# Kernel tuning notes

Measured on AMD Instinct MI355X. Metric: run time of the kernel, lower is better.

Reference implementation:

```python
import jax, jax.numpy as jnp
import numpy as np

N_NODES = 50000
N_EDGES = 800000
H = 4


def setup_inputs() -> dict:
    key = jax.random.key(0)
    ks = jax.random.split(key, 12)
    s = 0.05
    return {
        "x_feat": jax.random.normal(ks[0], (N_NODES, 128), jnp.float32),
        "W_fc": jax.random.normal(ks[1], (128, 256), jnp.float32) * s,
        "W1": jax.random.normal(ks[2], (256, 256), jnp.float32) * s,
        "al1": jax.random.normal(ks[3], (H, 64), jnp.float32) * s,
        "ar1": jax.random.normal(ks[4], (H, 64), jnp.float32) * s,
        "b1": jnp.zeros((256,), jnp.float32),
        "W2": jax.random.normal(ks[5], (256, 256), jnp.float32) * s,
        "al2": jax.random.normal(ks[6], (H, 64), jnp.float32) * s,
        "ar2": jax.random.normal(ks[7], (H, 64), jnp.float32) * s,
        "b2": jnp.zeros((256,), jnp.float32),
        "src": jax.random.randint(ks[8], (N_EDGES,), 0, N_NODES, jnp.int64 if jax.config.jax_enable_x64 else jnp.int32),
        "dst": jax.random.randint(ks[9], (N_EDGES,), 0, N_NODES, jnp.int64 if jax.config.jax_enable_x64 else jnp.int32),
    }


def _gat_layer(x, src, dst, W, attn_l, attn_r, bias, n_nodes):
    """DGL GATConv: project, per-edge leaky-relu scores, edge softmax by dst,
    weighted segment-sum, + bias, ELU. Returns [N, H, dh]."""
    h, dh = attn_l.shape
    feat = (x @ W).reshape(n_nodes, h, dh)            # [N,H,dh]
    el = jnp.einsum('nhd,hd->nh', feat, attn_l)        # [N,H]
    er = jnp.einsum('nhd,hd->nh', feat, attn_r)        # [N,H]
    e = jax.nn.leaky_relu(el[src] + er[dst], 0.2)      # [E,H]
    # numerically stable segment softmax over incoming edges of each dst
    m = jax.ops.segment_max(e, dst, num_segments=n_nodes)
    ex = jnp.exp(e - m[dst])
    z = jax.ops.segment_sum(ex, dst, num_segments=n_nodes)
    a = ex / z[dst]                                    # [E,H]
    msg = feat[src] * a[:, :, None]                    # [E,H,dh]
    out = jax.ops.segment_sum(msg, dst, num_segments=n_nodes)  # [N,H,dh]
    out = out + bias.reshape(h, dh)
    return jax.nn.elu(out)


def reference(x_feat, W_fc, W1, al1, ar1, b1, W2, al2, ar2, b2, src, dst):
    n = x_feat.shape[0]
    h = jnp.tanh(x_feat @ W_fc)                         # [N,256] (dropout = identity in eval)
    g1 = _gat_layer(h, src, dst, W1, al1, ar1, b1, n)   # [N,4,64]
    g1 = g1.reshape(n, -1)                              # [N,256]
    g2 = _gat_layer(g1, src, dst, W2, al2, ar2, b2, n)  # [N,4,64]
    return jnp.mean(g2, axis=-2)                        # mean over heads -> [N,64]
```

## Files before the change

kernel.cpp:

```cpp
#include <hip/hip_runtime.h>
#include <hip/hip_bf16.h>
#include <hip/hip_fp16.h>
#include <math.h>


typedef __attribute__((ext_vector_type(8))) short bf16x8;
typedef __attribute__((ext_vector_type(4))) float f32x4;

typedef const __attribute__((address_space(1))) char gas_char;
typedef __attribute__((address_space(3))) char las_char;

__device__ __forceinline__ void gload16(const void* g, void* l) {
    __builtin_amdgcn_global_load_lds((gas_char*)g, (las_char*)l, 16, 0, 0);
}

__device__ __forceinline__ void split2(float v, short& h, short& l) {
    __hip_bfloat16 bh = __float2bfloat16(v);
    float r = v - __bfloat162float(bh);
    __hip_bfloat16 bl = __float2bfloat16(r);
    h = *reinterpret_cast<short*>(&bh);
    l = *reinterpret_cast<short*>(&bl);
}

__device__ __forceinline__ float fast_tanh(float x) {
    x = fminf(fmaxf(x, -15.f), 15.f);
    float e = __expf(2.f * x);
    return (e - 1.f) * __builtin_amdgcn_rcpf(e + 1.f);
}

__device__ __forceinline__ float leaky02(float x) { return x > 0.f ? x : 0.2f * x; }

__device__ __forceinline__ float sel_head(float4 q, int h) {
    float lo = (h & 1) ? q.y : q.x;
    float hi = (h & 1) ? q.w : q.z;
    return (h & 2) ? hi : lo;
}

__global__ __launch_bounds__(256) void wsplit3_kernel(
        const float* __restrict__ W0, short* __restrict__ B0h, short* __restrict__ B0l,
        const float* __restrict__ W1, short* __restrict__ B1h, short* __restrict__ B1l,
        const float* __restrict__ W2, short* __restrict__ B2h, short* __restrict__ B2l) {
    int idx = blockIdx.x * 256 + threadIdx.x;
    const float* W;
    short *Bh, *Bl;
    int K, rel;
    if (idx < 128 * 256) {
        W = W0; Bh = B0h; Bl = B0l; K = 128; rel = idx;
    } else if (idx < 128 * 256 + 256 * 256) {
        W = W1; Bh = B1h; Bl = B1l; K = 256; rel = idx - 128 * 256;
    } else if (idx < 128 * 256 + 2 * 256 * 256) {
        W = W2; Bh = B2h; Bl = B2l; K = 256; rel = idx - 128 * 256 - 256 * 256;
    } else {
        return;
    }
    int k = rel >> 8, n = rel & 255;
    short h, l;
    split2(W[rel], h, l);
    Bh[n * K + k] = h;
    Bl[n * K + k] = l;
}

__global__ __launch_bounds__(256) void xsplit_kernel(const float* __restrict__ X,
                                                     short* __restrict__ Xh,
                                                     short* __restrict__ Xl, int total) {
    int idx = blockIdx.x * 256 + threadIdx.x;
    if (idx >= total) return;
    short h, l;
    split2(X[idx], h, l);
    Xh[idx] = h;
    Xl[idx] = l;
}

template<int K, bool TANH, bool ELER, bool SPLIT_OUT>
__global__ __launch_bounds__(256, 2) void mfma_gemm_kernel(
        const short* __restrict__ Ah, const short* __restrict__ Al,
        const short* __restrict__ Bh, const short* __restrict__ Bl,
        short* __restrict__ Oh, short* __restrict__ Ol, __half* __restrict__ O16,
        int M,
        const float* __restrict__ al, const float* __restrict__ ar,
        float* __restrict__ el, float* __restrict__ er) {
    __shared__ __align__(16) short As_h[2][128 * 32];
    __shared__ __align__(16) short As_l[2][128 * 32];
    __shared__ __align__(16) short Bs_h[2][128 * 32];
    __shared__ __align__(16) short Bs_l[2][128 * 32];

    const int tid = threadIdx.x;
    const int row0 = blockIdx.x * 128;
    const int col0 = blockIdx.y * 128;

    const int lane = tid & 63;
    const int lr = lane & 15;
    const int lg = lane >> 4;
    const int wid = tid >> 6;
    const int wm = wid >> 1;
    const int wn = wid & 1;

    const int srow = wid * 32 + (lane >> 2);
    const int scol = (lane & 3) * 8;
    const size_t aoff1 = (size_t)(row0 + srow) * K + scol;
    const size_t aoff2 = aoff1 + (size_t)16 * K;
    const size_t boff1 = (size_t)(col0 + srow) * K + scol;
    const size_t boff2 = boff1 + (size_t)16 * K;
    const int lbase1 = (wid * 32) * 32;
    const int lbase2 = (wid * 32 + 16) * 32;

    auto stage = [&](int buf, int k0) {
        gload16(Ah + aoff1 + k0, &As_h[buf][lbase1]);
        gload16(Ah + aoff2 + k0, &As_h[buf][lbase2]);
        gload16(Al + aoff1 + k0, &As_l[buf][lbase1]);
        gload16(Al + aoff2 + k0, &As_l[buf][lbase2]);
        gload16(Bh + boff1 + k0, &Bs_h[buf][lbase1]);
        gload16(Bh + boff2 + k0, &Bs_h[buf][lbase2]);
        gload16(Bl + boff1 + k0, &Bs_l[buf][lbase1]);
        gload16(Bl + boff2 + k0, &Bs_l[buf][lbase2]);
    };

    f32x4 acc[4][4];
#pragma unroll
    for (int i = 0; i < 4; ++i)
#pragma unroll
        for (int j = 0; j < 4; ++j) acc[i][j] = (f32x4){0.f, 0.f, 0.f, 0.f};

    constexpr int NT = K / 32;
    stage(0, 0);
    __syncthreads();

    int cur = 0;
#pragma unroll
    for (int t = 0; t < NT; ++t) {
        if (t + 1 < NT) stage(cur ^ 1, (t + 1) * 32);

        bf16x8 ah[4], av[4], bh[4], bv[4];
#pragma unroll
        for (int q = 0; q < 4; ++q) {
            int arow = (wm * 64 + q * 16 + lr) * 32 + lg * 8;
            int brow = (wn * 64 + q * 16 + lr) * 32 + lg * 8;
            ah[q] = *reinterpret_cast<const bf16x8*>(&As_h[cur][arow]);
            av[q] = *reinterpret_cast<const bf16x8*>(&As_l[cur][arow]);
            bh[q] = *reinterpret_cast<const bf16x8*>(&Bs_h[cur][brow]);
            bv[q] = *reinterpret_cast<const bf16x8*>(&Bs_l[cur][brow]);
        }
#pragma unroll
        for (int mt = 0; mt < 4; ++mt)
#pragma unroll
            for (int nt = 0; nt < 4; ++nt) {
                acc[mt][nt] = __builtin_amdgcn_mfma_f32_16x16x32_bf16(ah[mt], bh[nt], acc[mt][nt], 0, 0, 0);
                acc[mt][nt] = __builtin_amdgcn_mfma_f32_16x16x32_bf16(ah[mt], bv[nt], acc[mt][nt], 0, 0, 0);
                acc[mt][nt] = __builtin_amdgcn_mfma_f32_16x16x32_bf16(av[mt], bh[nt], acc[mt][nt], 0, 0, 0);
            }
        __syncthreads();
        cur ^= 1;
    }

    const int head = blockIdx.y * 2 + wn;
    float alv[4], arv[4];
    if (ELER) {
#pragma unroll
        for (int nt = 0; nt < 4; ++nt) {
            alv[nt] = al[head * 64 + nt * 16 + lr];
            arv[nt] = ar[head * 64 + nt * 16 + lr];
        }
    }
#pragma unroll
    for (int mt = 0; mt < 4; ++mt) {
#pragma unroll
        for (int r = 0; r < 4; ++r) {
            int row = row0 + wm * 64 + mt * 16 + lg * 4 + r;
            bool valid = row < M;
            float sl = 0.f, sr_ = 0.f;
#pragma unroll
            for (int nt = 0; nt < 4; ++nt) {
                float v = acc[mt][nt][r];
                if (TANH) v = fast_tanh(v);
                if (valid) {
                    size_t ci = (size_t)row * 256 + col0 + wn * 64 + nt * 16 + lr;
                    if (SPLIT_OUT) {
                        short hh, ll;
                        split2(v, hh, ll);
                        Oh[ci] = hh;
                        Ol[ci] = ll;
                    } else {
                        O16[ci] = __float2half(v);
                    }
                }
                if (ELER) { sl = fmaf(v, alv[nt], sl); sr_ = fmaf(v, arv[nt], sr_); }
            }
            if (ELER) {
#pragma unroll
                for (int mask = 1; mask < 16; mask <<= 1) {
                    sl  += __shfl_xor(sl, mask, 16);
                    sr_ += __shfl_xor(sr_, mask, 16);
                }
                if (valid && lr == 0) {
                    el[row * 4 + head] = sl;
                    er[row * 4 + head] = sr_;
                }
            }
        }
    }
}

__global__ void count_deg_kernel(const int* __restrict__ dst, int* __restrict__ deg, int E) {
    int i = blockIdx.x * blockDim.x + threadIdx.x;
    if (i < E) atomicAdd(&deg[dst[i]], 1);
}

__global__ __launch_bounds__(1024) void scan_kernel(const int* __restrict__ deg,
                                                    int* __restrict__ offs,
                                                    int* __restrict__ cursor, int n) {
    __shared__ int wsum[16];
    const int tid = threadIdx.x, lane = tid & 63, wv = tid >> 6;
    int carry = 0;
    for (int base = 0; base < n; base += 4096) {
        int i = base + tid * 4;
        int v0 = 0, v1 = 0, v2 = 0, v3 = 0;
        if (i + 3 < n) {
            int4 q = *reinterpret_cast<const int4*>(&deg[i]);
            v0 = q.x; v1 = q.y; v2 = q.z; v3 = q.w;
        } else if (i < n) {
            v0 = deg[i];
            if (i + 1 < n) v1 = deg[i + 1];
            if (i + 2 < n) v2 = deg[i + 2];
        }
        int s = v0 + v1 + v2 + v3;
        int incl = s;
#pragma unroll
        for (int d = 1; d < 64; d <<= 1) {
            int t = __shfl_up(incl, d, 64);
            if (lane >= d) incl += t;
        }
        if (lane == 63) wsum[wv] = incl;
        __syncthreads();
        int woff = 0, tot = 0;
#pragma unroll
        for (int w2 = 0; w2 < 16; ++w2) {
            int x = wsum[w2];
            if (w2 < wv) woff += x;
            tot += x;
        }
        int excl = carry + woff + incl - s;
        if (i < n) {
            int p0 = excl, p1 = p0 + v0, p2 = p1 + v1, p3 = p2 + v2;
            offs[i] = p0; cursor[i] = p0;
            if (i + 1 < n) { offs[i + 1] = p1; cursor[i + 1] = p1; }
            if (i + 2 < n) { offs[i + 2] = p2; cursor[i + 2] = p2; }
            if (i + 3 < n) { offs[i + 3] = p3; cursor[i + 3] = p3; }
        }
        carry += tot;
        __syncthreads();
    }
    if (tid == 0) offs[n] = carry;
}

__global__ void fill_csr_kernel(const int* __restrict__ src, const int* __restrict__ dst,
                                int* __restrict__ cursor, int* __restrict__ srcs_sorted,
                                int* __restrict__ dsts_sorted, int E) {
    int i = blockIdx.x * blockDim.x + threadIdx.x;
    if (i < E) {
        int d = dst[i];
        int pos = atomicAdd(&cursor[d], 1);
        srcs_sorted[pos] = src[i];
        dsts_sorted[pos] = d;
    }
}

__global__ __launch_bounds__(256) void edge_w_kernel(const int* __restrict__ srcs,
                                                     const int* __restrict__ dsts,
                                                     const float* __restrict__ el,
                                                     const float* __restrict__ er,
                                                     float4* __restrict__ w, int E) {
    int i = blockIdx.x * 256 + threadIdx.x;
    if (i >= E) return;
    int s = srcs[i], d = dsts[i];
    const float4 a = *reinterpret_cast<const float4*>(&el[(size_t)s * 4]);
    const float4 b = *reinterpret_cast<const float4*>(&er[(size_t)d * 4]);
    float4 o;
    o.x = __expf(leaky02(a.x + b.x));
    o.y = __expf(leaky02(a.y + b.y));
    o.z = __expf(leaky02(a.z + b.z));
    o.w = __expf(leaky02(a.w + b.w));
    w[i] = o;
}

template<bool FINAL>
__global__ __launch_bounds__(256) void gat_agg_kernel(const __half* __restrict__ feat,
                                                      const float4* __restrict__ wq,
                                                      const int* __restrict__ srcs,
                                                      const int* __restrict__ offs,
                                                      const float* __restrict__ bias,
                                                      float* __restrict__ out,
                                                      short* __restrict__ Gh,
                                                      short* __restrict__ Gl, int N) {
    const int tid = threadIdx.x;
    const int w = tid >> 6, l = tid & 63;
    const int n = blockIdx.x * 4 + w;
    if (n >= N) return;
    const int h = l >> 4;
    const int begin = offs[n];
    const int deg = offs[n + 1] - begin;
    const __half* fbase = feat + (size_t)l * 4;
    const float4 zero4 = make_float4(0.f, 0.f, 0.f, 0.f);

    float4 acc = zero4;
    float z = 0.f;

    for (int j = 0; j < deg; j += 8) {
        const int rem = deg - j;
        const int nb = __builtin_amdgcn_readfirstlane(begin + j);
        const int s0 = srcs[nb + 0];
        const int s1 = (rem > 1) ? srcs[nb + 1] : 0;
        const int s2 = (rem > 2) ? srcs[nb + 2] : 0;
        const int s3 = (rem > 3) ? srcs[nb + 3] : 0;
        const int s4 = (rem > 4) ? srcs[nb + 4] : 0;
        const int s5 = (rem > 5) ? srcs[nb + 5] : 0;
        const int s6 = (rem > 6) ? srcs[nb + 6] : 0;
        const int s7 = (rem > 7) ? srcs[nb + 7] : 0;
        const float4 w0 = wq[nb + 0];
        const float4 w1 = (rem > 1) ? wq[nb + 1] : zero4;
        const float4 w2 = (rem > 2) ? wq[nb + 2] : zero4;
        const float4 w3 = (rem > 3) ? wq[nb + 3] : zero4;
        const float4 w4 = (rem > 4) ? wq[nb + 4] : zero4;
        const float4 w5 = (rem > 5) ? wq[nb + 5] : zero4;
        const float4 w6 = (rem > 6) ? wq[nb + 6] : zero4;
        const float4 w7 = (rem > 7) ? wq[nb + 7] : zero4;
        const uint2 u0 = *reinterpret_cast<const uint2*>(fbase + (size_t)s0 * 256);
        const uint2 u1 = *reinterpret_cast<const uint2*>(fbase + (size_t)s1 * 256);
        const uint2 u2 = *reinterpret_cast<const uint2*>(fbase + (size_t)s2 * 256);
        const uint2 u3 = *reinterpret_cast<const uint2*>(fbase + (size_t)s3 * 256);
        const uint2 u4 = *reinterpret_cast<const uint2*>(fbase + (size_t)s4 * 256);
        const uint2 u5 = *reinterpret_cast<const uint2*>(fbase + (size_t)s5 * 256);
        const uint2 u6 = *reinterpret_cast<const uint2*>(fbase + (size_t)s6 * 256);
        const uint2 u7 = *reinterpret_cast<const uint2*>(fbase + (size_t)s7 * 256);

        const float e0 = sel_head(w0, h);
        const float e1 = sel_head(w1, h);
        const float e2 = sel_head(w2, h);
        const float e3 = sel_head(w3, h);
        const float e4 = sel_head(w4, h);
        const float e5 = sel_head(w5, h);
        const float e6 = sel_head(w6, h);
        const float e7 = sel_head(w7, h);
        z += ((e0 + e1) + (e2 + e3)) + ((e4 + e5) + (e6 + e7));

        auto fma4 = [&](float e, uint2 u) {
            const __half2* hp = reinterpret_cast<const __half2*>(&u);
            float2 a = __half22float2(hp[0]);
            float2 b = __half22float2(hp[1]);
            acc.x = fmaf(e, a.x, acc.x); acc.y = fmaf(e, a.y, acc.y);
            acc.z = fmaf(e, b.x, acc.z); acc.w = fmaf(e, b.y, acc.w);
        };
        fma4(e0, u0); fma4(e1, u1); fma4(e2, u2); fma4(e3, u3);
        fma4(e4, u4); fma4(e5, u5); fma4(e6, u6); fma4(e7, u7);
    }

    const float rz = (z > 0.f) ? __builtin_amdgcn_rcpf(z) : 0.f;
    const float4 bv = *reinterpret_cast<const float4*>(&bias[l * 4]);
    float4 v;
    v.x = fmaf(acc.x, rz, bv.x);
    v.y = fmaf(acc.y, rz, bv.y);
    v.z = fmaf(acc.z, rz, bv.z);
    v.w = fmaf(acc.w, rz, bv.w);
    v.x = v.x > 0.f ? v.x : expm1f(v.x);
    v.y = v.y > 0.f ? v.y : expm1f(v.y);
    v.z = v.z > 0.f ? v.z : expm1f(v.z);
    v.w = v.w > 0.f ? v.w : expm1f(v.w);

    if (!FINAL) {
        short4 hh, ll;
        split2(v.x, hh.x, ll.x);
        split2(v.y, hh.y, ll.y);
        split2(v.z, hh.z, ll.z);
        split2(v.w, hh.w, ll.w);
        *reinterpret_cast<short4*>(&Gh[(size_t)n * 256 + l * 4]) = hh;
        *reinterpret_cast<short4*>(&Gl[(size_t)n * 256 + l * 4]) = ll;
    } else {
        v.x += __shfl_down(v.x, 32, 64); v.y += __shfl_down(v.y, 32, 64);
        v.z += __shfl_down(v.z, 32, 64); v.w += __shfl_down(v.w, 32, 64);
        v.x += __shfl_down(v.x, 16, 64); v.y += __shfl_down(v.y, 16, 64);
        v.z += __shfl_down(v.z, 16, 64); v.w += __shfl_down(v.w, 16, 64);
        if (l < 16) {
            float4 o;
            o.x = 0.25f * v.x; o.y = 0.25f * v.y; o.z = 0.25f * v.z; o.w = 0.25f * v.w;
            *reinterpret_cast<float4*>(&out[(size_t)n * 64 + l * 4]) = o;
        }
    }
}

extern "C" void kernel_launch(void* const* d_in, const int* in_sizes, int n_in,
                              void* d_out, int out_size, void* d_ws, size_t ws_size,
                              hipStream_t stream) {
    const float* x_feat = (const float*)d_in[0];
    const float* W_fc   = (const float*)d_in[1];
    const float* W1     = (const float*)d_in[2];
    const float* al1    = (const float*)d_in[3];
    const float* ar1    = (const float*)d_in[4];
    const float* b1     = (const float*)d_in[5];
    const float* W2     = (const float*)d_in[6];
    const float* al2    = (const float*)d_in[7];
    const float* ar2    = (const float*)d_in[8];
    const float* b2     = (const float*)d_in[9];
    const int*   src    = (const int*)d_in[10];
    const int*   dst    = (const int*)d_in[11];
    float* out = (float*)d_out;

    const int N = in_sizes[0] / 128;
    const int E = in_sizes[10];
    const int NB = (N + 127) / 128;
    const int M_pad = NB * 128;

    char* ws = (char*)d_ws;
    size_t off = 0;
    auto alloc = [&](size_t bytes) -> void* {
        off = (off + 255) & ~(size_t)255;
        void* p = ws + off;
        off += bytes;
        return p;
    };
    short* Xh   = (short*)alloc((size_t)M_pad * 128 * 2);
    short* Xl   = (short*)alloc((size_t)M_pad * 128 * 2);
    short* Hh   = (short*)alloc((size_t)M_pad * 256 * 2);
    short* Hl   = (short*)alloc((size_t)M_pad * 256 * 2);
    __half* f16 = (__half*)alloc((size_t)M_pad * 256 * 2);
    float* el   = (float*)alloc((size_t)N * 4 * 4);
    float* er   = (float*)alloc((size_t)N * 4 * 4);
    int* deg    = (int*)alloc((size_t)N * 4);
    int* offs   = (int*)alloc((size_t)(N + 4) * 4);
    int* cursor = (int*)alloc((size_t)N * 4);
    int* srcs_sorted = (int*)alloc((size_t)(E + 8) * 4);
    int* dsts_sorted = (int*)alloc((size_t)(E + 8) * 4);
    float4* wq  = (float4*)alloc((size_t)(E + 8) * 16);
    short* Bfc_h = (short*)alloc((size_t)256 * 128 * 2);
    short* Bfc_l = (short*)alloc((size_t)256 * 128 * 2);
    short* B1_h  = (short*)alloc((size_t)256 * 256 * 2);
    short* B1_l  = (short*)alloc((size_t)256 * 256 * 2);
    short* B2_h  = (short*)alloc((size_t)256 * 256 * 2);
    short* B2_l  = (short*)alloc((size_t)256 * 256 * 2);

    const int eb = (E + 255) / 256;
    dim3 ggrid(NB, 2);
    const int agrid = (N + 3) / 4;

    hipMemsetAsync(deg, 0, (size_t)N * 4, stream);
    count_deg_kernel<<<eb, 256, 0, stream>>>(dst, deg, E);
    scan_kernel<<<1, 1024, 0, stream>>>(deg, offs, cursor, N);
    fill_csr_kernel<<<eb, 256, 0, stream>>>(src, dst, cursor, srcs_sorted, dsts_sorted, E);

    wsplit3_kernel<<<(128 * 256 + 2 * 256 * 256 + 255) / 256, 256, 0, stream>>>(
        W_fc, Bfc_h, Bfc_l, W1, B1_h, B1_l, W2, B2_h, B2_l);
    xsplit_kernel<<<(N * 128 + 255) / 256, 256, 0, stream>>>(x_feat, Xh, Xl, N * 128);

    mfma_gemm_kernel<128, true, false, true><<<ggrid, 256, 0, stream>>>(
        Xh, Xl, Bfc_h, Bfc_l, Hh, Hl, nullptr, N, nullptr, nullptr, nullptr, nullptr);
    mfma_gemm_kernel<256, false, true, false><<<ggrid, 256, 0, stream>>>(
        Hh, Hl, B1_h, B1_l, nullptr, nullptr, f16, N, al1, ar1, el, er);
    edge_w_kernel<<<eb, 256, 0, stream>>>(srcs_sorted, dsts_sorted, el, er, wq, E);
    gat_agg_kernel<false><<<agrid, 256, 0, stream>>>(
        f16, wq, srcs_sorted, offs, b1, nullptr, Hh, Hl, N);
    mfma_gemm_kernel<256, false, true, false><<<ggrid, 256, 0, stream>>>(
        Hh, Hl, B2_h, B2_l, nullptr, nullptr, f16, N, al2, ar2, el, er);
    edge_w_kernel<<<eb, 256, 0, stream>>>(srcs_sorted, dsts_sorted, el, er, wq, E);
    gat_agg_kernel<true><<<agrid, 256, 0, stream>>>(
        f16, wq, srcs_sorted, offs, b2, out, nullptr, nullptr, N);
}
```

Measured before the change: 475.5 us.

## Fuse edge-weight computation into aggregation and merge prep kernels

Removes the separate edge_w kernel and computes exp(leaky_relu(el[src]+er[dst])) inline in the aggregation loop, gathering el per source and loading er once per destination. This drops the per-edge float4 weight buffer and the dsts_sorted array, saving their writes and reads. The x split, weight split and degree zeroing move into one prep kernel with vectorized float4 x conversion, replacing a memset and two launches. In exchange the aggregation does extra random 16-byte el gathers and recomputes exp per lane, with four lanes of each head doing duplicate work.

```diff
diff --git a/kernel.cpp b/kernel.cpp
--- a/kernel.cpp
+++ b/kernel.cpp
@@ -36,20 +36,36 @@
     return (h & 2) ? hi : lo;
 }
 
-__global__ __launch_bounds__(256) void wsplit3_kernel(
+__global__ __launch_bounds__(256) void prep_kernel(
+        const float* __restrict__ X, short* __restrict__ Xh, short* __restrict__ Xl,
+        int xquads,
         const float* __restrict__ W0, short* __restrict__ B0h, short* __restrict__ B0l,
         const float* __restrict__ W1, short* __restrict__ B1h, short* __restrict__ B1l,
-        const float* __restrict__ W2, short* __restrict__ B2h, short* __restrict__ B2l) {
-    int idx = blockIdx.x * 256 + threadIdx.x;
+        const float* __restrict__ W2, short* __restrict__ B2h, short* __restrict__ B2l,
+        int* __restrict__ deg, int N) {
+    int gid = blockIdx.x * 256 + threadIdx.x;
+    if (gid < N) deg[gid] = 0;
+    if (gid < xquads) {
+        float4 v = reinterpret_cast<const float4*>(X)[gid];
+        short4 h, l;
+        split2(v.x, h.x, l.x);
+        split2(v.y, h.y, l.y);
+        split2(v.z, h.z, l.z);
+        split2(v.w, h.w, l.w);
+        reinterpret_cast<short4*>(Xh)[gid] = h;
+        reinterpret_cast<short4*>(Xl)[gid] = l;
+        return;
+    }
+    int rel = gid - xquads;
     const float* W;
     short *Bh, *Bl;
-    int K, rel;
-    if (idx < 128 * 256) {
-        W = W0; Bh = B0h; Bl = B0l; K = 128; rel = idx;
-    } else if (idx < 128 * 256 + 256 * 256) {
-        W = W1; Bh = B1h; Bl = B1l; K = 256; rel = idx - 128 * 256;
-    } else if (idx < 128 * 256 + 2 * 256 * 256) {
-        W = W2; Bh = B2h; Bl = B2l; K = 256; rel = idx - 128 * 256 - 256 * 256;
+    int K;
+    if (rel < 128 * 256) {
+        W = W0; Bh = B0h; Bl = B0l; K = 128;
+    } else if (rel < 128 * 256 + 256 * 256) {
+        W = W1; Bh = B1h; Bl = B1l; K = 256; rel -= 128 * 256;
+    } else if (rel < 128 * 256 + 2 * 256 * 256) {
+        W = W2; Bh = B2h; Bl = B2l; K = 256; rel -= 128 * 256 + 256 * 256;
     } else {
         return;
     }
@@ -58,17 +74,6 @@
     split2(W[rel], h, l);
     Bh[n * K + k] = h;
     Bl[n * K + k] = l;
-}
-
-__global__ __launch_bounds__(256) void xsplit_kernel(const float* __restrict__ X,
-                                                     short* __restrict__ Xh,
-                                                     short* __restrict__ Xl, int total) {
-    int idx = blockIdx.x * 256 + threadIdx.x;
-    if (idx >= total) return;
-    short h, l;
-    split2(X[idx], h, l);
-    Xh[idx] = h;
-    Xl[idx] = l;
 }
 
 template<int K, bool TANH, bool ELER, bool SPLIT_OUT>
@@ -253,38 +258,19 @@
 }
 
 __global__ void fill_csr_kernel(const int* __restrict__ src, const int* __restrict__ dst,
-                                int* __restrict__ cursor, int* __restrict__ srcs_sorted,
-                                int* __restrict__ dsts_sorted, int E) {
+                                int* __restrict__ cursor, int* __restrict__ srcs_sorted, int E) {
     int i = blockIdx.x * blockDim.x + threadIdx.x;
     if (i < E) {
         int d = dst[i];
         int pos = atomicAdd(&cursor[d], 1);
         srcs_sorted[pos] = src[i];
-        dsts_sorted[pos] = d;
-    }
-}
-
-__global__ __launch_bounds__(256) void edge_w_kernel(const int* __restrict__ srcs,
-                                                     const int* __restrict__ dsts,
-                                                     const float* __restrict__ el,
-                                                     const float* __restrict__ er,
-                                                     float4* __restrict__ w, int E) {
-    int i = blockIdx.x * 256 + threadIdx.x;
-    if (i >= E) return;
-    int s = srcs[i], d = dsts[i];
-    const float4 a = *reinterpret_cast<const float4*>(&el[(size_t)s * 4]);
-    const float4 b = *reinterpret_cast<const float4*>(&er[(size_t)d * 4]);
-    float4 o;
-    o.x = __expf(leaky02(a.x + b.x));
-    o.y = __expf(leaky02(a.y + b.y));
-    o.z = __expf(leaky02(a.z + b.z));
-    o.w = __expf(leaky02(a.w + b.w));
-    w[i] = o;
+    }
 }
 
 template<bool FINAL>
 __global__ __launch_bounds__(256) void gat_agg_kernel(const __half* __restrict__ feat,
-                                                      const float4* __restrict__ wq,
+                                                      const float* __restrict__ el,
+                                                      const float* __restrict__ er,
                                                       const int* __restrict__ srcs,
                                                       const int* __restrict__ offs,
                                                       const float* __restrict__ bias,
@@ -298,10 +284,10 @@
     const int h = l >> 4;
     const int begin = offs[n];
     const int deg = offs[n + 1] - begin;
+    const float erh = er[n * 4 + h];
     const __half* fbase = feat + (size_t)l * 4;
-    const float4 zero4 = make_float4(0.f, 0.f, 0.f, 0.f);
-
-    float4 acc = zero4;
+
+    float4 acc = make_float4(0.f, 0.f, 0.f, 0.f);
     float z = 0.f;
 
     for (int j = 0; j < deg; j += 8) {
@@ -315,14 +301,14 @@
         const int s5 = (rem > 5) ? srcs[nb + 5] : 0;
         const int s6 = (rem > 6) ? srcs[nb + 6] : 0;
         const int s7 = (rem > 7) ? srcs[nb + 7] : 0;
-        const float4 w0 = wq[nb + 0];
-        const float4 w1 = (rem > 1) ? wq[nb + 1] : zero4;
-        const float4 w2 = (rem > 2) ? wq[nb + 2] : zero4;
-        const float4 w3 = (rem > 3) ? wq[nb + 3] : zero4;
-        const float4 w4 = (rem > 4) ? wq[nb + 4] : zero4;
-        const float4 w5 = (rem > 5) ? wq[nb + 5] : zero4;
-        const float4 w6 = (rem > 6) ? wq[nb + 6] : zero4;
-        const float4 w7 = (rem > 7) ? wq[nb + 7] : zero4;
+        const float4 q0 = *reinterpret_cast<const float4*>(&el[(size_t)s0 * 4]);
+        const float4 q1 = *reinterpret_cast<const float4*>(&el[(size_t)s1 * 4]);
+        const float4 q2 = *reinterpret_cast<const float4*>(&el[(size_t)s2 * 4]);
+        const float4 q3 = *reinterpret_cast<const float4*>(&el[(size_t)s3 * 4]);
+        const float4 q4 = *reinterpret_cast<const float4*>(&el[(size_t)s4 * 4]);
+        const float4 q5 = *reinterpret_cast<const float4*>(&el[(size_t)s5 * 4]);
+        const float4 q6 = *reinterpret_cast<const float4*>(&el[(size_t)s6 * 4]);
+        const float4 q7 = *reinterpret_cast<const float4*>(&el[(size_t)s7 * 4]);
         const uint2 u0 = *reinterpret_cast<const uint2*>(fbase + (size_t)s0 * 256);
         const uint2 u1 = *reinterpret_cast<const uint2*>(fbase + (size_t)s1 * 256);
         const uint2 u2 = *reinterpret_cast<const uint2*>(fbase + (size_t)s2 * 256);
@@ -332,14 +318,14 @@
         const uint2 u6 = *reinterpret_cast<const uint2*>(fbase + (size_t)s6 * 256);
         const uint2 u7 = *reinterpret_cast<const uint2*>(fbase + (size_t)s7 * 256);
 
-        const float e0 = sel_head(w0, h);
-        const float e1 = sel_head(w1, h);
-        const float e2 = sel_head(w2, h);
-        const float e3 = sel_head(w3, h);
-        const float e4 = sel_head(w4, h);
-        const float e5 = sel_head(w5, h);
-        const float e6 = sel_head(w6, h);
-        const float e7 = sel_head(w7, h);
+        const float e0 = __expf(leaky02(sel_head(q0, h) + erh));
+        const float e1 = (rem > 1) ? __expf(leaky02(sel_head(q1, h) + erh)) : 0.f;
+        const float e2 = (rem > 2) ? __expf(leaky02(sel_head(q2, h) + erh)) : 0.f;
+        const float e3 = (rem > 3) ? __expf(leaky02(sel_head(q3, h) + erh)) : 0.f;
+        const float e4 = (rem > 4) ? __expf(leaky02(sel_head(q4, h) + erh)) : 0.f;
+        const float e5 = (rem > 5) ? __expf(leaky02(sel_head(q5, h) + erh)) : 0.f;
+        const float e6 = (rem > 6) ? __expf(leaky02(sel_head(q6, h) + erh)) : 0.f;
+        const float e7 = (rem > 7) ? __expf(leaky02(sel_head(q7, h) + erh)) : 0.f;
         z += ((e0 + e1) + (e2 + e3)) + ((e4 + e5) + (e6 + e7));
 
         auto fma4 = [&](float e, uint2 u) {
@@ -427,8 +413,6 @@
     int* offs   = (int*)alloc((size_t)(N + 4) * 4);
     int* cursor = (int*)alloc((size_t)N * 4);
     int* srcs_sorted = (int*)alloc((size_t)(E + 8) * 4);
-    int* dsts_sorted = (int*)alloc((size_t)(E + 8) * 4);
-    float4* wq  = (float4*)alloc((size_t)(E + 8) * 16);
     short* Bfc_h = (short*)alloc((size_t)256 * 128 * 2);
     short* Bfc_l = (short*)alloc((size_t)256 * 128 * 2);
     short* B1_h  = (short*)alloc((size_t)256 * 256 * 2);
@@ -440,25 +424,22 @@
     dim3 ggrid(NB, 2);
     const int agrid = (N + 3) / 4;
 
-    hipMemsetAsync(deg, 0, (size_t)N * 4, stream);
+    const int xquads = N * 128 / 4;
+    const int prep_threads = xquads + 128 * 256 + 2 * 256 * 256;
+    prep_kernel<<<(prep_threads + 255) / 256, 256, 0, stream>>>(
+        x_feat, Xh, Xl, xquads, W_fc, Bfc_h, Bfc_l, W1, B1_h, B1_l, W2, B2_h, B2_l,
+        deg, N);
     count_deg_kernel<<<eb, 256, 0, stream>>>(dst, deg, E);
     scan_kernel<<<1, 1024, 0, stream>>>(deg, offs, cursor, N);
-    fill_csr_kernel<<<eb, 256, 0, stream>>>(src, dst, cursor, srcs_sorted, dsts_sorted, E);
-
-    wsplit3_kernel<<<(128 * 256 + 2 * 256 * 256 + 255) / 256, 256, 0, stream>>>(
-        W_fc, Bfc_h, Bfc_l, W1, B1_h, B1_l, W2, B2_h, B2_l);
-    xsplit_kernel<<<(N * 128 + 255) / 256, 256, 0, stream>>>(x_feat, Xh, Xl, N * 128);
-
+    fill_csr_kernel<<<eb, 256, 0, stream>>>(src, dst, cursor, srcs_sorted, E);
     mfma_gemm_kernel<128, true, false, true><<<ggrid, 256, 0, stream>>>(
         Xh, Xl, Bfc_h, Bfc_l, Hh, Hl, nullptr, N, nullptr, nullptr, nullptr, nullptr);
     mfma_gemm_kernel<256, false, true, false><<<ggrid, 256, 0, stream>>>(
         Hh, Hl, B1_h, B1_l, nullptr, nullptr, f16, N, al1, ar1, el, er);
-    edge_w_kernel<<<eb, 256, 0, stream>>>(srcs_sorted, dsts_sorted, el, er, wq, E);
     gat_agg_kernel<false><<<agrid, 256, 0, stream>>>(
-        f16, wq, srcs_sorted, offs, b1, nullptr, Hh, Hl, N);
+        f16, el, er, srcs_sorted, offs, b1, nullptr, Hh, Hl, N);
     mfma_gemm_kernel<256, false, true, false><<<ggrid, 256, 0, stream>>>(
         Hh, Hl, B2_h, B2_l, nullptr, nullptr, f16, N, al2, ar2, el, er);
-    edge_w_kernel<<<eb, 256, 0, stream>>>(srcs_sorted, dsts_sorted, el, er, wq, E);
     gat_agg_kernel<true><<<agrid, 256, 0, stream>>>(
-        f16, wq, srcs_sorted, offs, b2, out, nullptr, nullptr, N);
-}
+        f16, el, er, srcs_sorted, offs, b2, out, nullptr, nullptr, N);
+}
```

Result: faster. 455.6 us (-4.2%).
